# Performance work log

Hardware: AMD Instinct MI355X
Metric: run time of the kernel (lower is better)

Reference implementation:

```python
import jax, jax.numpy as jnp
import numpy as np

B, T, E = 2, 2048, 2048
H, HKV, DH = 16, 8, 128
G = H // HKV
WINDOW = 512
ROPE_THETA = 10000.0
EPS = 1e-6


def _rms_norm(x, w):
    # Gemma3RMSNorm: fp32 rms_norm with weight = 1 + w
    xf = x.astype(jnp.float32)
    y = xf * jax.lax.rsqrt(jnp.mean(xf * xf, axis=-1, keepdims=True) + EPS)
    return (y * (1.0 + w.astype(jnp.float32))).astype(x.dtype)


def _rotate_half(x):
    x1, x2 = x[..., : DH // 2], x[..., DH // 2 :]
    return jnp.concatenate((-x2, x1), axis=-1)


def setup_inputs() -> dict:
    key = jax.random.key(0)
    ks = jax.random.split(key, 5)
    s = 0.02
    return {
        "x": jax.random.normal(ks[0], (B, T, E), jnp.float32),
        "wq": jax.random.normal(ks[1], (H * DH, E), jnp.float32) * s,
        "wk": jax.random.normal(ks[2], (HKV * DH, E), jnp.float32) * s,
        "wv": jax.random.normal(ks[3], (HKV * DH, E), jnp.float32) * s,
        "wo": jax.random.normal(ks[4], (E, H * DH), jnp.float32) * s,
        "q_norm_w": jnp.zeros((DH,), jnp.float32),
        "k_norm_w": jnp.zeros((DH,), jnp.float32),
    }


def reference(x, wq, wk, wv, wo, q_norm_w, k_norm_w):
    # projections: [B,T,H,DH] -> [B,H,T,DH]
    q = (x @ wq.T).reshape(B, T, H, DH).transpose(0, 2, 1, 3)
    k = (x @ wk.T).reshape(B, T, HKV, DH).transpose(0, 2, 1, 3)
    v = (x @ wv.T).reshape(B, T, HKV, DH).transpose(0, 2, 1, 3)

    # QK-RMSNorm over head_dim
    q = _rms_norm(q, q_norm_w)
    k = _rms_norm(k, k_norm_w)

    # RoPE (prefill: positions 0..T-1)
    pos = jnp.arange(T, dtype=jnp.float32)
    inv_freq = 1.0 / (ROPE_THETA ** (jnp.arange(0, DH, 2, dtype=jnp.float32) / DH))
    freqs = pos[:, None] * inv_freq[None, :]          # [T, DH//2]
    emb = jnp.concatenate((freqs, freqs), axis=-1)    # [T, DH]
    cos = jnp.cos(emb)[None, None, :, :]
    sin = jnp.sin(emb)[None, None, :, :]
    q = q * cos + _rotate_half(q) * sin
    k = k * cos + _rotate_half(k) * sin

    # GQA attention with causal + sliding-window mask, fp32 scores
    q = q * (DH ** -0.5)
    qg = q.reshape(B, HKV, G, T, DH)
    att = jnp.einsum("bhgtd,bhkd->bhgtk", qg.astype(jnp.float32), k.astype(jnp.float32))

    dist = jnp.arange(T)[:, None] - jnp.arange(T)[None, :]   # [T, T]
    mask = (dist >= 0) & (dist <= WINDOW)
    att = jnp.where(mask[None, None, None, :, :], att, jnp.finfo(jnp.float32).min)
    att = jax.nn.softmax(att, axis=-1).astype(q.dtype)

    ctx = jnp.einsum("bhgtk,bhkd->bhgtd", att, v)
    out = ctx.reshape(B, H, T, DH).transpose(0, 2, 1, 3).reshape(B, T, H * DH)
    return out @ wo.T
```

## Files before the change

kernel.cpp:

```cpp
#include <hip/hip_runtime.h>
#include <hip/hip_bf16.h>
#include <stdint.h>

#define B_ 2
#define T_ 2048
#define E_ 2048
#define H_ 16
#define HKV_ 8
#define DH_ 128
#define WINDOW_ 512

typedef unsigned short ush;
typedef float f32x4 __attribute__((ext_vector_type(4)));
typedef __bf16 bf16x8 __attribute__((ext_vector_type(8)));
typedef uint32_t u32x4 __attribute__((ext_vector_type(4)));

static __device__ __forceinline__ ush f2bf(float f) {
    uint32_t u = __float_as_uint(f);
    uint32_t r = (u + 0x7fffu + ((u >> 16) & 1u)) >> 16;
    return (ush)r;
}
static __device__ __forceinline__ float bf2f(ush h) {
    return __uint_as_float(((uint32_t)h) << 16);
}

__global__ __launch_bounds__(256) void cast_all(const float* __restrict__ x,
        const float* __restrict__ wq, const float* __restrict__ wk,
        const float* __restrict__ wv, const float* __restrict__ wo,
        ush* __restrict__ dst) {
    const int stride = gridDim.x * blockDim.x;
    for (int i = blockIdx.x * blockDim.x + threadIdx.x; i < 5242880; i += stride) {
        const float4* src;
        if (i < 2097152)      src = (const float4*)x  + i;
        else if (i < 3145728) src = (const float4*)wq + (i - 2097152);
        else if (i < 3670016) src = (const float4*)wk + (i - 3145728);
        else if (i < 4194304) src = (const float4*)wv + (i - 3670016);
        else                  src = (const float4*)wo + (i - 4194304);
        const float4 f = *src;
        ushort4 o;
        o.x = f2bf(f.x); o.y = f2bf(f.y); o.z = f2bf(f.z); o.w = f2bf(f.w);
        reinterpret_cast<ushort4*>(dst)[i] = o;
    }
}

template <int MODE>
__global__ __launch_bounds__(512, 2) void gemm_bt3(
    const ush* __restrict__ A, const ush* __restrict__ Bm,
    float* __restrict__ Cf, ush* __restrict__ q, ush* __restrict__ k, ush* __restrict__ vT,
    int M, int N, int K)
{
    __shared__ ush As[3][128 * 64];
    __shared__ ush Bs[3][256 * 64];
    const int tid = threadIdx.x;
    const int lane = tid & 63;
    const int wid = tid >> 6;
    const int wr = wid >> 2, wc = wid & 3;
    const int g = lane >> 4, t = lane & 15;
    const int gm0 = blockIdx.x * 128, gn0 = blockIdx.y * 256;

    f32x4 acc[4][4] = {};

    auto stageA2 = [&](int kt, int m3) {
#pragma unroll
        for (int i = 0; i < 2; ++i) {
            const int C = i * 512 + tid;
            const int r = C >> 3, c = C & 7;
            const ush* src = A + (size_t)(gm0 + r) * K + (kt << 6) + ((c ^ (r & 7)) << 3);
            __builtin_amdgcn_global_load_lds(
                (const __attribute__((address_space(1))) void*)src,
                (__attribute__((address_space(3))) void*)(&As[m3][C << 3]), 16, 0, 0);
        }
    };
    auto stageB4 = [&](int kt, int m3) {
#pragma unroll
        for (int i = 0; i < 4; ++i) {
            const int C = i * 512 + tid;
            const int r = C >> 3, c = C & 7;
            const ush* src = Bm + (size_t)(gn0 + r) * K + (kt << 6) + ((c ^ (r & 7)) << 3);
            __builtin_amdgcn_global_load_lds(
                (const __attribute__((address_space(1))) void*)src,
                (__attribute__((address_space(3))) void*)(&Bs[m3][C << 3]), 16, 0, 0);
        }
    };

    const int nt = K >> 6;

    stageA2(0, 0); stageB4(0, 0);
    stageA2(1, 1); stageB4(1, 1);
    asm volatile("s_waitcnt vmcnt(6)" ::: "memory");
    __builtin_amdgcn_s_barrier();
    __builtin_amdgcn_sched_barrier(0);

    int m3 = 0;
    for (int kt = 0; kt < nt; ++kt) {
        const int st3 = (m3 + 2 >= 3) ? m3 - 1 : m3 + 2;
        bf16x8 af[4][2], bfr[4][2];

#pragma unroll
        for (int mf = 0; mf < 4; ++mf)
#pragma unroll
            for (int ks = 0; ks < 2; ++ks) {
                const int row = wr * 64 + mf * 16 + t;
                af[mf][ks] = *reinterpret_cast<const bf16x8*>(
                    &As[m3][row * 64 + ((((ks << 2) + g) ^ (t & 7)) << 3)]);
            }
#pragma unroll
        for (int nf = 0; nf < 4; ++nf)
#pragma unroll
            for (int ks = 0; ks < 2; ++ks) {
                const int row = wc * 64 + nf * 16 + t;
                bfr[nf][ks] = *reinterpret_cast<const bf16x8*>(
                    &Bs[m3][row * 64 + ((((ks << 2) + g) ^ (t & 7)) << 3)]);
            }

        if (kt + 2 < nt) { stageA2(kt + 2, st3); stageB4(kt + 2, st3); }

        __builtin_amdgcn_s_setprio(1);
#pragma unroll
        for (int ks = 0; ks < 2; ++ks)
#pragma unroll
            for (int mf = 0; mf < 4; ++mf)
#pragma unroll
                for (int nf = 0; nf < 4; ++nf)
                    acc[mf][nf] = __builtin_amdgcn_mfma_f32_16x16x32_bf16(
                        af[mf][ks], bfr[nf][ks], acc[mf][nf], 0, 0, 0);
        __builtin_amdgcn_s_setprio(0);

        if (kt + 1 < nt) {
            if (kt + 2 < nt) asm volatile("s_waitcnt vmcnt(6)" ::: "memory");
            else             asm volatile("s_waitcnt vmcnt(0)" ::: "memory");
        }
        __builtin_amdgcn_s_barrier();
        __builtin_amdgcn_sched_barrier(0);

        m3 = (m3 + 1 >= 3) ? 0 : m3 + 1;
    }

    const int rsub = (lane >> 4) << 2;
    const int csub = lane & 15;
#pragma unroll
    for (int mf = 0; mf < 4; ++mf) {
        const int row0 = gm0 + wr * 64 + mf * 16 + rsub;
#pragma unroll
        for (int nf = 0; nf < 4; ++nf) {
            const int col = gn0 + wc * 64 + nf * 16 + csub;
#pragma unroll
            for (int r = 0; r < 4; ++r) {
                const int row = row0 + r;
                if (MODE == 1) {
                    Cf[(size_t)row * N + col] = acc[mf][nf][r];
                } else {
                    const int bb = row >> 11, tt = row & (T_ - 1);
                    const ush val = f2bf(acc[mf][nf][r]);
                    if (col < H_ * DH_) {
                        const int hh = col >> 7, d = col & 127;
                        q[((((size_t)bb * H_ + hh) * T_ + tt) << 7) + d] = val;
                    } else if (col < H_ * DH_ + HKV_ * DH_) {
                        const int c2 = col - H_ * DH_;
                        const int hh = c2 >> 7, d = c2 & 127;
                        k[((((size_t)bb * HKV_ + hh) * T_ + tt) << 7) + d] = val;
                    } else {
                        const int c2 = col - H_ * DH_ - HKV_ * DH_;
                        const int hh = c2 >> 7, d = c2 & 127;
                        vT[((size_t)((bb * HKV_ + hh) * DH_ + d) << 11) + tt] = val;
                    }
                }
            }
        }
    }
}

__global__ __launch_bounds__(256) void norm_rope(ush* __restrict__ q, ush* __restrict__ k,
                                                 const float* __restrict__ qw,
                                                 const float* __restrict__ kw)
{
    const int lane = threadIdx.x & 63;
    const int row = blockIdx.x * 4 + (threadIdx.x >> 6);
    const int NQ = B_ * H_ * T_;
    ush* p; const float* w; int t; bool isq = (row < NQ);
    if (isq) { p = q + ((size_t)row << 7); t = row & (T_ - 1); w = qw; }
    else     { int r2 = row - NQ; p = k + ((size_t)r2 << 7); t = r2 & (T_ - 1); w = kw; }

    float x0 = bf2f(p[lane]);
    float x1 = bf2f(p[lane + 64]);
    float ss = x0 * x0 + x1 * x1;
#pragma unroll
    for (int off = 32; off; off >>= 1) ss += __shfl_xor(ss, off);
    const float rms = rsqrtf(ss * (1.0f / 128.0f) + 1e-6f);
    float y0 = x0 * rms * (1.0f + w[lane]);
    float y1 = x1 * rms * (1.0f + w[lane + 64]);

    const float invf = expf(-(float)lane * 0.14391156831212787f);
    const float fr = (float)t * invf;
    const float c = cosf(fr), s = sinf(fr);
    float o0 = y0 * c - y1 * s;
    float o1 = y1 * c + y0 * s;
    if (isq) { o0 *= 0.08838834764831845f; o1 *= 0.08838834764831845f; }
    p[lane] = f2bf(o0);
    p[lane + 64] = f2bf(o1);
}

__global__ __launch_bounds__(256) void attn_mfma(const ush* __restrict__ q,
        const ush* __restrict__ k, const ush* __restrict__ vT, ush* __restrict__ ctx)
{
    __shared__ ush Ks[2][32 * 128];
    __shared__ ush Vs[2][128 * 32];
    const int tid = threadIdx.x;
    const int lane = tid & 63;
    const int w = tid >> 6;
    const int g = lane >> 4;
    const int t = lane & 15;

    int bi = blockIdx.x;
    bi = (bi & 7) * 128 + (bi >> 3);
    const int qtile = bi & 31;
    const int hh = (bi >> 5) & 15;
    const int b = bi >> 9;
    const int qb = qtile * 64;
    const int hkv = hh >> 1;

    const ush* qptr = q + ((((size_t)b * H_ + hh) * T_ + qb) << 7);
    const ush* kbase = k + (((size_t)b * HKV_ + hkv) << 18);
    const ush* vtbase = vT + (((size_t)b * HKV_ + hkv) << 18);

    bf16x8 qf[4];
#pragma unroll
    for (int c = 0; c < 4; ++c)
        qf[c] = *reinterpret_cast<const bf16x8*>(qptr + ((16 * w + t) << 7) + 32 * c + 8 * g);

    const int kstart = (qb >= WINDOW_) ? (qb - WINDOW_) : 0;
    const int nt = (qb + 64 - kstart) >> 5;

    auto stage = [&](int ti, int buf) {
        const int kt0 = kstart + (ti << 5);
#pragma unroll
        for (int i = 0; i < 2; ++i) {
            const int C = w * 128 + i * 64 + lane;
            {
                const int row = C >> 4, ch = C & 15;
                const ush* gk = kbase + ((size_t)(kt0 + row) << 7) + ch * 8;
                __builtin_amdgcn_global_load_lds(
                    (const __attribute__((address_space(1))) void*)gk,
                    (__attribute__((address_space(3))) void*)(&Ks[buf][(w * 128 + i * 64) * 8]),
                    16, 0, 0);
            }
            {
                const int row = C >> 2, ch = C & 3;
                const ush* gv = vtbase + ((size_t)row << 11) + kt0 + ch * 8;
                __builtin_amdgcn_global_load_lds(
                    (const __attribute__((address_space(1))) void*)gv,
                    (__attribute__((address_space(3))) void*)(&Vs[buf][(w * 128 + i * 64) * 8]),
                    16, 0, 0);
            }
        }
    };

    float m = -1e30f, lsum = 0.f;
    f32x4 o[8] = {};

    stage(0, 0);
    __syncthreads();

    for (int ti = 0; ti < nt; ++ti) {
        const int cur = ti & 1;
        if (ti + 1 < nt) stage(ti + 1, cur ^ 1);
        const int kt0 = kstart + (ti << 5);
        const int qw0 = qb + 16 * w;
        const bool active = (kt0 + 31 >= qw0 - WINDOW_) && (kt0 <= qw0 + 15);
        if (active) {
            f32x4 st[2] = {};
#pragma unroll
            for (int s = 0; s < 2; ++s)
#pragma unroll
                for (int c = 0; c < 4; ++c) {
                    bf16x8 kf = *reinterpret_cast<const bf16x8*>(
                        &Ks[cur][(16 * s + t) * 128 + 32 * c + 8 * g]);
                    st[s] = __builtin_amdgcn_mfma_f32_16x16x32_bf16(kf, qf[c], st[s], 0, 0, 0);
                }
            const int tg = qb + 16 * w + t;
            float e[2][4];
            float mymax = -3e38f;
#pragma unroll
            for (int s = 0; s < 2; ++s)
#pragma unroll
                for (int r = 0; r < 4; ++r) {
                    const int key = kt0 + 16 * s + 4 * g + r;
                    const int dist = tg - key;
                    const bool valid = (dist >= 0) && (dist <= WINDOW_);
                    const float sv = valid ? st[s][r] : -3e38f;
                    e[s][r] = sv;
                    mymax = fmaxf(mymax, sv);
                }
            mymax = fmaxf(mymax, __shfl_xor(mymax, 16));
            mymax = fmaxf(mymax, __shfl_xor(mymax, 32));
            const float mn = fmaxf(m, mymax);
            const float sc = __expf(m - mn);
            float esum = 0.f;
#pragma unroll
            for (int s = 0; s < 2; ++s)
#pragma unroll
                for (int r = 0; r < 4; ++r) {
                    const float ev = __expf(e[s][r] - mn);
                    e[s][r] = ev;
                    esum += ev;
                }
            esum += __shfl_xor(esum, 16);
            esum += __shfl_xor(esum, 32);
            lsum = lsum * sc + esum;
            m = mn;
#pragma unroll
            for (int ds = 0; ds < 8; ++ds) {
                o[ds][0] *= sc; o[ds][1] *= sc; o[ds][2] *= sc; o[ds][3] *= sc;
            }
            uint32_t word[2][2];
#pragma unroll
            for (int s = 0; s < 2; ++s)
#pragma unroll
                for (int wd = 0; wd < 2; ++wd)
                    word[s][wd] = (uint32_t)f2bf(e[s][2 * wd])
                                | ((uint32_t)f2bf(e[s][2 * wd + 1]) << 16);
            u32x4 bw;
#pragma unroll
            for (int e2 = 0; e2 < 4; ++e2) {
                const int srcl = 16 * (2 * (g & 1) + (e2 >> 1)) + t;
                const uint32_t v0 = __shfl(word[0][e2 & 1], srcl);
                const uint32_t v1 = __shfl(word[1][e2 & 1], srcl);
                bw[e2] = (g >= 2) ? v1 : v0;
            }
            const bf16x8 pF = __builtin_bit_cast(bf16x8, bw);
#pragma unroll
            for (int ds = 0; ds < 8; ++ds) {
                bf16x8 vtF = *reinterpret_cast<const bf16x8*>(
                    &Vs[cur][(16 * ds + t) * 32 + 8 * g]);
                o[ds] = __builtin_amdgcn_mfma_f32_16x16x32_bf16(vtF, pF, o[ds], 0, 0, 0);
            }
        }
        __syncthreads();
    }

    const float linv = 1.0f / lsum;
    ush* cptr = ctx + (((size_t)b * T_ + qb + 16 * w + t) * (H_ * DH_)) + hh * DH_;
#pragma unroll
    for (int ds = 0; ds < 8; ++ds) {
        ushort4 pk;
        pk.x = f2bf(o[ds][0] * linv);
        pk.y = f2bf(o[ds][1] * linv);
        pk.z = f2bf(o[ds][2] * linv);
        pk.w = f2bf(o[ds][3] * linv);
        *reinterpret_cast<ushort4*>(cptr + 16 * ds + 4 * g) = pk;
    }
}

extern "C" void kernel_launch(void* const* d_in, const int* in_sizes, int n_in,
                              void* d_out, int out_size, void* d_ws, size_t ws_size,
                              hipStream_t stream)
{
    const float* x   = (const float*)d_in[0];
    const float* wq  = (const float*)d_in[1];
    const float* wk  = (const float*)d_in[2];
    const float* wv  = (const float*)d_in[3];
    const float* wo  = (const float*)d_in[4];
    const float* qnw = (const float*)d_in[5];
    const float* knw = (const float*)d_in[6];
    float* out = (float*)d_out;

    ush* ws    = (ush*)d_ws;
    ush* xbf   = ws;
    ush* wqkv  = xbf  + 8388608;
    ush* wobf  = wqkv + 8388608;
    ush* qraw  = wobf + 4194304;
    ush* kraw  = qraw + 8388608;
    ush* vTb   = kraw + 4194304;
    ush* ctx   = vTb  + 4194304;

    cast_all<<<2048, 256, 0, stream>>>(x, wq, wk, wv, wo, ws);

    gemm_bt3<0><<<dim3(32, 16), 512, 0, stream>>>(xbf, wqkv, nullptr, qraw, kraw, vTb,
                                                  4096, 4096, 2048);
    norm_rope<<<(65536 + 32768) / 4, 256, 0, stream>>>(qraw, kraw, qnw, knw);
    attn_mfma<<<1024, 256, 0, stream>>>(qraw, kraw, vTb, ctx);
    gemm_bt3<1><<<dim3(32, 8), 512, 0, stream>>>(ctx, wobf, out, nullptr, nullptr, nullptr,
                                                 4096, 2048, 2048);
    (void)in_sizes; (void)n_in; (void)out_size; (void)ws_size;
}
```

Baseline: 236.8 us.

## Use 256x256 tiles with double buffering and swizzled block order for QKV GEMM

Splits the templated GEMM into a dedicated QKV kernel and an output-projection kernel. The QKV kernel grows the block tile from 128x256 to 256x256 with 8x4 accumulator fragments per wave, switches from triple to double buffering with a full vmcnt(0) wait each step, remaps block indices for L2 locality, and raises wave priority around the MFMA loop. The aim is more operand reuse per global load and better cache reuse. In exchange it uses more registers and 128KB of LDS, leaving one block per CU and only 256 blocks, and it overlaps loads less than the triple-buffered pipeline did.

```diff
diff --git a/kernel.cpp b/kernel.cpp
--- a/kernel.cpp
+++ b/kernel.cpp
@@ -43,11 +43,124 @@
     }
 }
 
-template <int MODE>
-__global__ __launch_bounds__(512, 2) void gemm_bt3(
+__global__ __launch_bounds__(512, 2) void gemm_qkv(
     const ush* __restrict__ A, const ush* __restrict__ Bm,
-    float* __restrict__ Cf, ush* __restrict__ q, ush* __restrict__ k, ush* __restrict__ vT,
-    int M, int N, int K)
+    ush* __restrict__ q, ush* __restrict__ k, ush* __restrict__ vT, int K)
+{
+    __shared__ ush As[2][256 * 64];
+    __shared__ ush Bs[2][256 * 64];
+    const int tid = threadIdx.x;
+    const int lane = tid & 63;
+    const int wid = tid >> 6;
+    const int wr = wid >> 2, wc = wid & 3;
+    const int g = lane >> 4, t = lane & 15;
+
+    const int r0 = blockIdx.y * 16 + blockIdx.x;
+    const int swz = (r0 & 7) * 32 + (r0 >> 3);
+    const int gm0 = (swz & 15) * 256;
+    const int gn0 = (swz >> 4) * 256;
+
+    f32x4 acc[8][4] = {};
+
+    auto stage = [&](int kt, int buf) {
+#pragma unroll
+        for (int i = 0; i < 4; ++i) {
+            const int C = i * 512 + tid;
+            const int r = C >> 3, c = C & 7;
+            const ush* src = A + (size_t)(gm0 + r) * K + (kt << 6) + ((c ^ (r & 7)) << 3);
+            __builtin_amdgcn_global_load_lds(
+                (const __attribute__((address_space(1))) void*)src,
+                (__attribute__((address_space(3))) void*)(&As[buf][C << 3]), 16, 0, 0);
+        }
+#pragma unroll
+        for (int i = 0; i < 4; ++i) {
+            const int C = i * 512 + tid;
+            const int r = C >> 3, c = C & 7;
+            const ush* src = Bm + (size_t)(gn0 + r) * K + (kt << 6) + ((c ^ (r & 7)) << 3);
+            __builtin_amdgcn_global_load_lds(
+                (const __attribute__((address_space(1))) void*)src,
+                (__attribute__((address_space(3))) void*)(&Bs[buf][C << 3]), 16, 0, 0);
+        }
+    };
+
+    const int nt = K >> 6;
+
+    stage(0, 0);
+    asm volatile("s_waitcnt vmcnt(0)" ::: "memory");
+    __builtin_amdgcn_s_barrier();
+    __builtin_amdgcn_sched_barrier(0);
+
+    for (int kt = 0; kt < nt; ++kt) {
+        const int buf = kt & 1;
+        if (kt + 1 < nt) stage(kt + 1, buf ^ 1);
+
+        bf16x8 bfr[4][2];
+#pragma unroll
+        for (int nf = 0; nf < 4; ++nf)
+#pragma unroll
+            for (int ks = 0; ks < 2; ++ks) {
+                const int row = wc * 64 + nf * 16 + t;
+                bfr[nf][ks] = *reinterpret_cast<const bf16x8*>(
+                    &Bs[buf][row * 64 + ((((ks << 2) + g) ^ (t & 7)) << 3)]);
+            }
+
+        __builtin_amdgcn_s_setprio(1);
+#pragma unroll
+        for (int mf = 0; mf < 8; ++mf) {
+            bf16x8 af[2];
+            const int row = wr * 128 + mf * 16 + t;
+#pragma unroll
+            for (int ks = 0; ks < 2; ++ks)
+                af[ks] = *reinterpret_cast<const bf16x8*>(
+                    &As[buf][row * 64 + ((((ks << 2) + g) ^ (t & 7)) << 3)]);
+#pragma unroll
+            for (int ks = 0; ks < 2; ++ks)
+#pragma unroll
+                for (int nf = 0; nf < 4; ++nf)
+                    acc[mf][nf] = __builtin_amdgcn_mfma_f32_16x16x32_bf16(
+                        af[ks], bfr[nf][ks], acc[mf][nf], 0, 0, 0);
+        }
+        __builtin_amdgcn_s_setprio(0);
+
+        if (kt + 1 < nt)
+            asm volatile("s_waitcnt vmcnt(0)" ::: "memory");
+        __builtin_amdgcn_s_barrier();
+        __builtin_amdgcn_sched_barrier(0);
+    }
+
+    const int rsub = (lane >> 4) << 2;
+    const int csub = lane & 15;
+#pragma unroll
+    for (int mf = 0; mf < 8; ++mf) {
+        const int row0 = gm0 + wr * 128 + mf * 16 + rsub;
+#pragma unroll
+        for (int nf = 0; nf < 4; ++nf) {
+            const int col = gn0 + wc * 64 + nf * 16 + csub;
+#pragma unroll
+            for (int r = 0; r < 4; ++r) {
+                const int row = row0 + r;
+                const int bb = row >> 11, tt = row & (T_ - 1);
+                const ush val = f2bf(acc[mf][nf][r]);
+                if (col < H_ * DH_) {
+                    const int hh = col >> 7, d = col & 127;
+                    q[((((size_t)bb * H_ + hh) * T_ + tt) << 7) + d] = val;
+                } else if (col < H_ * DH_ + HKV_ * DH_) {
+                    const int c2 = col - H_ * DH_;
+                    const int hh = c2 >> 7, d = c2 & 127;
+                    k[((((size_t)bb * HKV_ + hh) * T_ + tt) << 7) + d] = val;
+                } else {
+                    const int c2 = col - H_ * DH_ - HKV_ * DH_;
+                    const int hh = c2 >> 7, d = c2 & 127;
+                    vT[((size_t)((bb * HKV_ + hh) * DH_ + d) << 11) + tt] = val;
+                }
+            }
+        }
+    }
+}
+
+__global__ __launch_bounds__(512, 2) void gemm_out(
+    const ush* __restrict__ A, const ush* __restrict__ Bm,
+    float* __restrict__ Cf, int M, int N, int K)
 {
     __shared__ ush As[3][128 * 64];
     __shared__ ush Bs[3][256 * 64];
@@ -95,7 +208,6 @@
     for (int kt = 0; kt < nt; ++kt) {
         const int st3 = (m3 + 2 >= 3) ? m3 - 1 : m3 + 2;
         bf16x8 af[4][2], bfr[4][2];
-
 #pragma unroll
         for (int mf = 0; mf < 4; ++mf)
 #pragma unroll
@@ -145,27 +257,8 @@
         for (int nf = 0; nf < 4; ++nf) {
             const int col = gn0 + wc * 64 + nf * 16 + csub;
 #pragma unroll
-            for (int r = 0; r < 4; ++r) {
-                const int row = row0 + r;
-                if (MODE == 1) {
-                    Cf[(size_t)row * N + col] = acc[mf][nf][r];
-                } else {
-                    const int bb = row >> 11, tt = row & (T_ - 1);
-                    const ush val = f2bf(acc[mf][nf][r]);
-                    if (col < H_ * DH_) {
-                        const int hh = col >> 7, d = col & 127;
-                        q[((((size_t)bb * H_ + hh) * T_ + tt) << 7) + d] = val;
-                    } else if (col < H_ * DH_ + HKV_ * DH_) {
-                        const int c2 = col - H_ * DH_;
-                        const int hh = c2 >> 7, d = c2 & 127;
-                        k[((((size_t)bb * HKV_ + hh) * T_ + tt) << 7) + d] = val;
-                    } else {
-                        const int c2 = col - H_ * DH_ - HKV_ * DH_;
-                        const int hh = c2 >> 7, d = c2 & 127;
-                        vT[((size_t)((bb * HKV_ + hh) * DH_ + d) << 11) + tt] = val;
-                    }
-                }
-            }
+            for (int r = 0; r < 4; ++r)
+                Cf[(size_t)(row0 + r) * N + col] = acc[mf][nf][r];
         }
     }
 }
@@ -375,11 +468,9 @@
 
     cast_all<<<2048, 256, 0, stream>>>(x, wq, wk, wv, wo, ws);
 
-    gemm_bt3<0><<<dim3(32, 16), 512, 0, stream>>>(xbf, wqkv, nullptr, qraw, kraw, vTb,
-                                                  4096, 4096, 2048);
+    gemm_qkv<<<dim3(16, 16), 512, 0, stream>>>(xbf, wqkv, qraw, kraw, vTb, 2048);
     norm_rope<<<(65536 + 32768) / 4, 256, 0, stream>>>(qraw, kraw, qnw, knw);
     attn_mfma<<<1024, 256, 0, stream>>>(qraw, kraw, vTb, ctx);
-    gemm_bt3<1><<<dim3(32, 8), 512, 0, stream>>>(ctx, wobf, out, nullptr, nullptr, nullptr,
-                                                 4096, 2048, 2048);
+    gemm_out<<<dim3(32, 8), 512, 0, stream>>>(ctx, wobf, out, 4096, 2048, 2048);
     (void)in_sizes; (void)n_in; (void)out_size; (void)ws_size;
 }
```

Result: no change. 236.2 us (-0.2%).
